# Kernel tuning notes

Measured on AMD Instinct MI355X. Metric: run time of the kernel, lower is better.

The kernel has to match this reference:

```python
import jax, jax.numpy as jnp
import numpy as np

ALPHA = 0.4  # LeakyReLU negative slope used by the GAT


def _gat_head(h, W, a):
    # h: [N, F], W: [F, Fp], a: [2*Fp]; adjacency is all-ones so no masking
    Wh = h @ W                                   # [N, Fp]
    Fp = W.shape[1]
    e = jax.nn.leaky_relu(Wh @ a[:Fp][:, None] + (Wh @ a[Fp:])[None, :], ALPHA)
    att = jax.nn.softmax(e, axis=-1)             # [N, N]
    return att @ Wh                              # [N, Fp]


def _gat(h, W_heads, a_heads, W_gout, a_gout):
    # multi-head GAT: concat elu(head outputs), then single output attention layer
    heads = jax.vmap(_gat_head, in_axes=(None, 0, 0))(h, W_heads, a_heads)  # [H, N, Fp]
    x = jax.nn.elu(heads).transpose(1, 0, 2).reshape(h.shape[0], -1)        # [N, H*Fp]
    return jax.nn.elu(_gat_head(x, W_gout, a_gout))                          # [N, Cg]


def setup_inputs() -> dict:
    key = jax.random.key(0)
    ks = jax.random.split(key, 20)
    bs, R, S = 4, 512, 54
    h, w = 100, 152
    fc_dim, convs_dim4 = 1024, 512
    Cg, H, So = 256, 4, 128
    Fp = Cg // H
    sc = lambda k, shp, s=0.05: jax.random.normal(k, shp, dtype=jnp.float32) * s
    return {
        'region_f': jax.random.normal(ks[0], (bs * R, fc_dim), dtype=jnp.float32),
        'stuff_f': jax.random.normal(ks[1], (bs, convs_dim4, h, w), dtype=jnp.float32),
        'semseg_score': jax.random.normal(ks[2], (bs, S, h, w), dtype=jnp.float32),
        'W_rin': sc(ks[3], (fc_dim, Cg)), 'b_rin': jnp.zeros((Cg,), jnp.float32),
        'W_sin': sc(ks[4], (convs_dim4, Cg)), 'b_sin': jnp.zeros((Cg,), jnp.float32),
        'W_heads': sc(ks[5], (H, Cg, Fp), 0.1), 'a_heads': sc(ks[6], (H, 2 * Fp), 0.1),
        'W_gout': sc(ks[7], (H * Fp, Cg), 0.1), 'a_gout': sc(ks[8], (2 * Cg,), 0.1),
        'W_rout': sc(ks[9], (Cg, Cg)), 'b_rout': jnp.zeros((Cg,), jnp.float32),
        'W_sout': sc(ks[10], (Cg, So)), 'b_sout': jnp.zeros((So,), jnp.float32),
        'W_seg': sc(ks[11], (convs_dim4 + So, S)), 'b_seg': jnp.zeros((S,), jnp.float32),
    }


def reference(region_f, stuff_f, semseg_score,
              W_rin, b_rin, W_sin, b_sin,
              W_heads, a_heads, W_gout, a_gout,
              W_rout, b_rout, W_sout, b_sout,
              W_seg, b_seg):
    bs, Cd, h, w = stuff_f.shape
    S = semseg_score.shape[1]
    R = region_f.shape[0] // bs
    Cg = W_rin.shape[1]

    # node construction
    region_nodes = region_f @ W_rin + b_rin                           # [bs*R, Cg]
    score_flat = semseg_score.reshape(bs, S, h * w)
    class_center = jnp.einsum('bsn,bcn->bsc',
                              jax.nn.softmax(score_flat, axis=-1),
                              stuff_f.reshape(bs, Cd, h * w))          # [bs, S, Cd]
    class_nodes = class_center @ W_sin + b_sin                         # [bs, S, Cg]

    # per-image dense GAT over region + stuff nodes (batched via vmap)
    nodes = jnp.concatenate([region_nodes.reshape(bs, R, Cg), class_nodes], axis=1)
    graph_nodes = jax.vmap(lambda x: _gat(x, W_heads, a_heads, W_gout, a_gout))(nodes)
    new_region, new_class = graph_nodes[:, :R], graph_nodes[:, R:]

    # new box features: concat of original region features and projected graph features
    new_region_f = jnp.concatenate(
        [region_f, new_region.reshape(bs * R, Cg) @ W_rout + b_rout], axis=-1)

    # new stuff features: scatter class nodes back to pixels via class softmax
    new_class_nodes = new_class @ W_sout + b_sout                      # [bs, S, So]
    attn = jax.nn.softmax(score_flat, axis=1)                          # softmax over classes
    new_stuff = jnp.einsum('bsn,bso->bon', attn, new_class_nodes)      # [bs, So, h*w]
    new_stuff = new_stuff.reshape(bs, -1, h, w)

    # 1x1 conv seg head + x4 bilinear upsample (align_corners=False)
    seg_in = jnp.concatenate([stuff_f, new_stuff], axis=1)
    seg = jnp.einsum('bchw,co->bohw', seg_in, W_seg) + b_seg[None, :, None, None]
    segments = jax.image.resize(seg, (bs, S, 4 * h, 4 * w), method='bilinear')
    return new_region_f, segments
```

## Files before the change

### kernel.cpp

```cpp
#include <hip/hip_runtime.h>

#define HW 15200
#define SSD 54
#define NBATCH 4
#define NNODE 566
#define NPAD 576
#define CGD 256
#define CDD 512
#define NSPLIT 25
#define KSPAN 608

typedef __attribute__((ext_vector_type(4))) float f32x4;
typedef __attribute__((ext_vector_type(8))) short bf16x8;
typedef unsigned short ushort_t;

#define BT_RIN   0
#define BT_SIN   262144
#define BT_HEADS 393216
#define BT_GOUT  458752
#define BT_ROUT  524288
#define BT_SOUT  589824
#define BT_SEG2  622592
#define BT_TOTAL 630784

static constexpr long OFF_P     = 0;
static constexpr long OFF_CC    = OFF_P     + (long)NBATCH*SSD*HW;
static constexpr long OFF_NODES = OFF_CC    + (long)NBATCH*64*CDD;
static constexpr long OFF_WH    = OFF_NODES + (long)NBATCH*NNODE*CGD;
static constexpr long OFF_S1    = OFF_WH    + (long)16*NNODE*64;
static constexpr long OFF_S2    = OFF_S1    + 16*NPAD;
static constexpr long OFF_X     = OFF_S2    + 16*NPAD;
static constexpr long OFF_WH2   = OFF_X     + (long)NBATCH*NNODE*CGD;
static constexpr long OFF_S1B   = OFF_WH2   + (long)NBATCH*NNODE*CGD;
static constexpr long OFF_S2B   = OFF_S1B   + NBATCH*NPAD;
static constexpr long OFF_G     = OFF_S2B   + NBATCH*NPAD;
static constexpr long OFF_SUMS  = OFF_G     + (long)NBATCH*NNODE*CGD;
static constexpr long OFF_BT    = OFF_SUMS  + 256;
static constexpr long OFF_ASEG  = OFF_BT    + (BT_TOTAL/2 + 8);
static constexpr long OFF_SEG   = OFF_ASEG  + (long)NBATCH*64*576/2;
static constexpr long OFF_RFB   = OFF_SEG   + (long)NBATCH*SSD*HW;
static constexpr long OFF_WCOMB = OFF_RFB   + 1048576;
static constexpr long OFF_B2    = OFF_WCOMB + 8192;
static constexpr long OFF_ATTNB = OFF_B2    + 64;

__device__ inline float lrelu04(float x){ return x >= 0.f ? x : 0.4f*x; }
__device__ inline float eluf(float x){ return x > 0.f ? x : __expf(x) - 1.f; }
__device__ inline ushort_t f2bf(float f){
    unsigned u = __float_as_uint(f);
    return (ushort_t)((u + 0x7FFFu + ((u >> 16) & 1u)) >> 16);
}
__device__ inline float bf2f(ushort_t u){ return __uint_as_float((unsigned)u << 16); }
__device__ inline bf16x8 pack8(float4 lo, float4 hi){
    union { bf16x8 v; ushort_t u[8]; } p;
    p.u[0]=f2bf(lo.x); p.u[1]=f2bf(lo.y); p.u[2]=f2bf(lo.z); p.u[3]=f2bf(lo.w);
    p.u[4]=f2bf(hi.x); p.u[5]=f2bf(hi.y); p.u[6]=f2bf(hi.z); p.u[7]=f2bf(hi.w);
    return p.v;
}

__global__ __launch_bounds__(512)
void softmax_p(const float* __restrict__ score, ushort_t* __restrict__ pb,
               float* __restrict__ sums, float* __restrict__ s1s2b_zero,
               float* __restrict__ ccp)
{
    int blk = blockIdx.x;
    int t = threadIdx.x;
    if (blk < 256) {
        int b = blk >> 6, s = blk & 63;
        ushort_t* prow = pb + ((long)b*64 + s)*HW;
        if (s >= SSD) {
            for (int i = t; i < HW; i += 512) prow[i] = 0;
            if (t == 0) sums[b*64 + s] = 1.f;
            return;
        }
        const float* row = score + ((long)b*SSD + s)*HW;
        __shared__ float red[8];
        float s_ = 0.f;
        for (int i = t; i < HW; i += 512) {
            float e = __expf(row[i]);
            s_ += e;
            prow[i] = f2bf(e);
        }
        #pragma unroll
        for (int off = 32; off >= 1; off >>= 1) s_ += __shfl_down(s_, off);
        if ((t & 63) == 0) red[t >> 6] = s_;
        __syncthreads();
        if (t == 0) {
            float tot = 0.f;
            #pragma unroll
            for (int u = 0; u < 8; ++u) tot += red[u];
            sums[b*64 + s] = tot;
        }
        return;
    }
    long gid = (long)(blk - 256)*512 + t;
    if (gid < 4608) { s1s2b_zero[gid] = 0.f; return; }
    gid -= 4608;
    if (gid < (long)NBATCH*64*CDD) ccp[gid] = 0.f;
}

__global__ __launch_bounds__(256)
void cc_prep(const ushort_t* __restrict__ pb, const float* __restrict__ stuff,
             ushort_t* __restrict__ sbout, float* __restrict__ ccp,
             const float* __restrict__ score, ushort_t* __restrict__ attnb,
             const float* __restrict__ rf, float* __restrict__ out_region,
             ushort_t* __restrict__ rfb,
             const float* __restrict__ W_seg, ushort_t* __restrict__ asegb,
             const float* __restrict__ W_rin, const float* __restrict__ W_sin,
             const float* __restrict__ W_heads, const float* __restrict__ W_gout,
             const float* __restrict__ W_rout, const float* __restrict__ W_sout,
             const float* __restrict__ b_sout,
             ushort_t* __restrict__ bt, ushort_t* __restrict__ wcomb,
             float* __restrict__ bias2)
{
    int bid = blockIdx.x;
    if (bid < 832) {
        int g = (bid >> 6) * 8 + (bid & 7);
        if (g >= NSPLIT*NBATCH) return;
        int nt = (bid >> 3) & 7;
        int ks = g >> 2, b = g & 3;

        int w = threadIdx.x >> 6, l = threadIdx.x & 63;
        int lr = l & 15, lk = l >> 4;
        int n0 = nt*64 + w*16;
        const ushort_t* Prow = pb + ((long)b*64 + lr)*HW;
        const float*    Srow = stuff + ((long)b*CDD + n0 + lr)*HW;
        ushort_t*       Sout = sbout + ((long)b*CDD + n0 + lr)*HW;
        f32x4 acc[4] = {};
        int kbeg = ks * KSPAN;
        for (int k0 = kbeg; k0 < kbeg + KSPAN; k0 += 32) {
            int kk = k0 + lk*8;
            float4 lo = *(const float4*)&Srow[kk];
            float4 hi = *(const float4*)&Srow[kk + 4];
            bf16x8 bfv = pack8(lo, hi);
            *(bf16x8*)&Sout[kk] = bfv;
            #pragma unroll
            for (int mi = 0; mi < 4; ++mi) {
                bf16x8 af = *(const bf16x8*)&Prow[(long)mi*16*HW + kk];
                acc[mi] = __builtin_amdgcn_mfma_f32_16x16x32_bf16(af, bfv, acc[mi], 0, 0, 0);
            }
        }
        int c = n0 + lr;
        #pragma unroll
        for (int mi = 0; mi < 4; ++mi)
            #pragma unroll
            for (int r = 0; r < 4; ++r) {
                int m = mi*16 + lk*4 + r;
                atomicAdd(&ccp[((long)b*64 + m)*CDD + c], acc[mi][r]);
            }
        return;
    }
    long gid = (long)(bid - 832) * 256 + threadIdx.x;
    if (gid < (long)NBATCH*HW) {
        int b = (int)(gid / HW), n = (int)(gid % HW);
        const float* sp = score + (long)b*SSD*HW + n;
        float v[SSD];
        float m = -1e30f;
        #pragma unroll
        for (int s = 0; s < SSD; ++s) { v[s] = sp[(long)s*HW]; m = fmaxf(m, v[s]); }
        float sum = 0.f;
        #pragma unroll
        for (int s = 0; s < SSD; ++s) { v[s] = __expf(v[s] - m); sum += v[s]; }
        float inv = 1.f / sum;
        ushort_t* ap = attnb + (long)b*64*HW + n;
        #pragma unroll
        for (int s = 0; s < SSD; ++s) ap[(long)s*HW] = f2bf(v[s] * inv);
        #pragma unroll
        for (int s = SSD; s < 64; ++s) ap[(long)s*HW] = 0;
        return;
    }
    gid -= (long)NBATCH*HW;
    if (gid < 524288) {
        long row = gid / 256, col = gid % 256;
        float4 v = reinterpret_cast<const float4*>(rf)[gid];
        reinterpret_cast<float4*>(out_region)[row*320 + col] = v;
        union { ushort_t u[4]; uint2 q; } pk;
        pk.u[0]=f2bf(v.x); pk.u[1]=f2bf(v.y); pk.u[2]=f2bf(v.z); pk.u[3]=f2bf(v.w);
        reinterpret_cast<uint2*>(rfb)[gid] = pk.q;
        return;
    }
    gid -= 524288;
    if (gid < 131072) {
        int b = (int)(gid >> 15);
        int r = (int)(gid & 32767);
        int o = r >> 9, k = r & 511;
        asegb[(long)b*36864 + (long)o*576 + k] = f2bf(o < SSD ? W_seg[k*SSD + o] : 0.f);
        return;
    }
    gid -= 131072;
    if (gid < BT_TOTAL) {
        int i = (int)gid;
        float v;
        if (i < BT_SIN)        { int j=i;            int n=j>>10, k=j&1023; v = W_rin[k*256+n]; }
        else if (i < BT_HEADS) { int j=i-BT_SIN;     int n=j>>9,  k=j&511;  v = W_sin[k*256+n]; }
        else if (i < BT_GOUT)  { int j=i-BT_HEADS;   int h=j>>14, r=j&16383; int f=r>>8, k=r&255;
                                 v = W_heads[(h*256+k)*64+f]; }
        else if (i < BT_ROUT)  { int j=i-BT_GOUT;    int n=j>>8,  k=j&255;  v = W_gout[k*256+n]; }
        else if (i < BT_SOUT)  { int j=i-BT_ROUT;    int n=j>>8,  k=j&255;  v = W_rout[k*256+n]; }
        else if (i < BT_SEG2)  { int j=i-BT_SOUT;    int n=j>>8,  k=j&255;  v = W_sout[k*128+n]; }
        else                   { int j=i-BT_SEG2;    int o=j>>7,  k=j&127;
                                 v = (o < SSD) ? W_seg[(512+k)*SSD + o] : 0.f; }
        bt[i] = f2bf(v);
        return;
    }
    gid -= BT_TOTAL;
    if (gid < 16384) {
        int od = (int)(gid >> 8), k = (int)(gid & 255);
        float v = 0.f;
        if (od < SSD)
            for (int o = 0; o < 128; ++o)
                v += W_sout[k*128 + o] * W_seg[(512+o)*SSD + od];
        wcomb[(long)od*256 + k] = f2bf(v);
        return;
    }
    gid -= 16384;
    if (gid < 64) {
        int od = (int)gid;
        float v = 0.f;
        if (od < SSD)
            for (int o = 0; o < 128; ++o)
                v += b_sout[o] * W_seg[(512+o)*SSD + od];
        bias2[od] = v;
    }
}

template<bool AF32, int OUTMODE>
__device__ __forceinline__
void mm_body(int bx, int by, int bz,
             const void* __restrict__ Ap, const ushort_t* __restrict__ Bt,
             void* __restrict__ Cp, const float* __restrict__ bias,
             int M, int N, int K, int lda, int ldc,
             long sA, int zdivA, long sB, int zmodB, long sC)
{
    int z = bz;
    int w = threadIdx.x >> 6, l = threadIdx.x & 63;
    int lr = l & 15, lk = l >> 4;
    int m0 = bx * 64 + w * 16;
    int n0 = by * 64;
    const ushort_t* bt = Bt + (long)(z % zmodB) * sB;
    int mload = min(m0 + lr, M - 1);
    const float*    Af = (const float*)Ap    + (long)(z / zdivA) * sA + (long)mload * lda;
    const ushort_t* Ab = (const ushort_t*)Ap + (long)(z / zdivA) * sA + (long)mload * lda;
    f32x4 acc[4] = {};

    #pragma unroll 2
    for (int k0 = 0; k0 < K; k0 += 32) {
        int kk = k0 + lk * 8;
        bf16x8 af;
        if (AF32) {
            float4 lo = *(const float4*)&Af[kk];
            float4 hi = *(const float4*)&Af[kk + 4];
            af = pack8(lo, hi);
        } else {
            af = *(const bf16x8*)&Ab[kk];
        }
        #pragma unroll
        for (int j = 0; j < 4; ++j) {
            bf16x8 bf = *(const bf16x8*)&bt[(long)(n0 + j*16 + lr) * K + kk];
            acc[j] = __builtin_amdgcn_mfma_f32_16x16x32_bf16(af, bf, acc[j], 0, 0, 0);
        }
    }

    #pragma unroll
    for (int j = 0; j < 4; ++j) {
        int n = n0 + j*16 + lr;
        float bb = bias ? bias[n] : 0.f;
        #pragma unroll
        for (int r = 0; r < 4; ++r) {
            int m = m0 + lk*4 + r;
            if (OUTMODE == 2) {
                float v = acc[j][r] + bb;
                ((ushort_t*)Cp)[(long)z * sC + (long)n * ldc + m] =
                    (m < M) ? f2bf(v) : (ushort_t)0;
            } else {
                if (m >= M) continue;
                float v = acc[j][r] + bb;
                if (OUTMODE == 0)
                    ((float*)Cp)[(long)z * sC + (long)m * ldc + n] = v;
                else
                    ((ushort_t*)Cp)[(long)z * sC + (long)m * ldc + n] = f2bf(v);
            }
        }
    }
}

__global__ __launch_bounds__(256)
void nodes_both(const ushort_t* __restrict__ rfb, const ushort_t* __restrict__ btRin,
                const float* __restrict__ ccp, const float* __restrict__ sums,
                const ushort_t* __restrict__ btSin, ushort_t* __restrict__ nodes,
                const float* __restrict__ b_rin, const float* __restrict__ b_sin)
{
    if (blockIdx.x < 8) {
        mm_body<false, 1>(blockIdx.x, blockIdx.y, blockIdx.z,
                          rfb, btRin, nodes, b_rin,
                          512, 256, 1024, 1024, 256, 512L*1024, 1, 0, 1, (long)NNODE*CGD);
        return;
    }
    int by = blockIdx.y, bz = blockIdx.z;
    int w = threadIdx.x >> 6, l = threadIdx.x & 63;
    int lr = l & 15, lk = l >> 4;
    int m0 = w * 16, n0 = by * 64;
    int mload = min(m0 + lr, SSD - 1);
    const float* Af = ccp + ((long)bz*64 + mload)*CDD;
    float inv = 1.f / sums[bz*64 + mload];
    f32x4 acc[4] = {};

    #pragma unroll 2
    for (int k0 = 0; k0 < CDD; k0 += 32) {
        int kk = k0 + lk * 8;
        float4 lo = *(const float4*)&Af[kk];
        float4 hi = *(const float4*)&Af[kk + 4];
        lo.x *= inv; lo.y *= inv; lo.z *= inv; lo.w *= inv;
        hi.x *= inv; hi.y *= inv; hi.z *= inv; hi.w *= inv;
        bf16x8 af = pack8(lo, hi);
        #pragma unroll
        for (int j = 0; j < 4; ++j) {
            bf16x8 bf = *(const bf16x8*)&btSin[(long)(n0 + j*16 + lr) * CDD + kk];
            acc[j] = __builtin_amdgcn_mfma_f32_16x16x32_bf16(af, bf, acc[j], 0, 0, 0);
        }
    }

    #pragma unroll
    for (int j = 0; j < 4; ++j) {
        int n = n0 + j*16 + lr;
        float bb = b_sin[n];
        #pragma unroll
        for (int r = 0; r < 4; ++r) {
            int m = m0 + lk*4 + r;
            if (m >= SSD) continue;
            nodes[(long)bz*NNODE*CGD + (long)(512 + m)*CGD + n] = f2bf(acc[j][r] + bb);
        }
    }
}

__global__ __launch_bounds__(256)
void wht_heads(const ushort_t* __restrict__ nodes, const ushort_t* __restrict__ btHeads,
               ushort_t* __restrict__ wht, const float* __restrict__ a_heads,
               float* __restrict__ s1, float* __restrict__ s2)
{
    int bx = blockIdx.x, z = blockIdx.y;
    int w = threadIdx.x >> 6, l = threadIdx.x & 63;
    int lr = l & 15, lk = l >> 4;
    int m0 = bx*64 + w*16;
    const ushort_t* bt = btHeads + (long)(z & 3) * (64L*256);
    int mload = min(m0 + lr, NNODE - 1);
    const ushort_t* Ab = nodes + (long)(z >> 2)*((long)NNODE*CGD) + (long)mload*CGD;
    f32x4 acc[4] = {};

    #pragma unroll 2
    for (int k0 = 0; k0 < 256; k0 += 32) {
        int kk = k0 + lk*8;
        bf16x8 af = *(const bf16x8*)&Ab[kk];
        #pragma unroll
        for (int j = 0; j < 4; ++j) {
            bf16x8 bf = *(const bf16x8*)&bt[(long)(j*16 + lr)*256 + kk];
            acc[j] = __builtin_amdgcn_mfma_f32_16x16x32_bf16(af, bf, acc[j], 0, 0, 0);
        }
    }

    const float* av = a_heads + (long)(z & 3)*128;
    ushort_t* Wout = wht + (long)z*(64L*NPAD);
    float p1[4] = {0.f,0.f,0.f,0.f}, p2[4] = {0.f,0.f,0.f,0.f};
    #pragma unroll
    for (int j = 0; j < 4; ++j) {
        int f = j*16 + lr;
        float c1 = av[f], c2 = av[64 + f];
        #pragma unroll
        for (int r = 0; r < 4; ++r) {
            int m = m0 + lk*4 + r;
            float v = acc[j][r];
            Wout[(long)f*NPAD + m] = (m < NNODE) ? f2bf(v) : (ushort_t)0;
            if (m < NNODE) { p1[r] += v*c1; p2[r] += v*c2; }
        }
    }
    #pragma unroll
    for (int r = 0; r < 4; ++r)
        #pragma unroll
        for (int off = 1; off < 16; off <<= 1) {
            p1[r] += __shfl_xor(p1[r], off);
            p2[r] += __shfl_xor(p2[r], off);
        }
    if (lr == 0) {
        #pragma unroll
        for (int r = 0; r < 4; ++r) {
            int m = m0 + lk*4 + r;
            if (m < NNODE) {
                s1[(long)z*NPAD + m] = p1[r];
                s2[(long)z*NPAD + m] = p2[r];
            }
        }
    }
}

__global__ __launch_bounds__(256)
void wht2_gout(const ushort_t* __restrict__ xbuf, const ushort_t* __restrict__ btGout,
               ushort_t* __restrict__ wht2, const float* __restrict__ a_gout,
               float* __restrict__ s1b, float* __restrict__ s2b)
{
    int bx = blockIdx.x, by = blockIdx.y, z = blockIdx.z;
    int w = threadIdx.x >> 6, l = threadIdx.x & 63;
    int lr = l & 15, lk = l >> 4;
    int m0 = bx*64 + w*16;
    int n0 = by*64;
    int mload = min(m0 + lr, NNODE - 1);
    const ushort_t* Ab = xbuf + (long)z*((long)NNODE*CGD) + (long)mload*CGD;
    f32x4 acc[4] = {};

    #pragma unroll 2
    for (int k0 = 0; k0 < 256; k0 += 32) {
        int kk = k0 + lk*8;
        bf16x8 af = *(const bf16x8*)&Ab[kk];
        #pragma unroll
        for (int j = 0; j < 4; ++j) {
            bf16x8 bf = *(const bf16x8*)&btGout[(long)(n0 + j*16 + lr)*256 + kk];
            acc[j] = __builtin_amdgcn_mfma_f32_16x16x32_bf16(af, bf, acc[j], 0, 0, 0);
        }
    }

    ushort_t* Wout = wht2 + (long)z*(256L*NPAD);
    float p1[4] = {0.f,0.f,0.f,0.f}, p2[4] = {0.f,0.f,0.f,0.f};
    #pragma unroll
    for (int j = 0; j < 4; ++j) {
        int f = n0 + j*16 + lr;
        float c1 = a_gout[f], c2 = a_gout[256 + f];
        #pragma unroll
        for (int r = 0; r < 4; ++r) {
            int m = m0 + lk*4 + r;
            float v = acc[j][r];
            Wout[(long)f*NPAD + m] = (m < NNODE) ? f2bf(v) : (ushort_t)0;
            if (m < NNODE) { p1[r] += v*c1; p2[r] += v*c2; }
        }
    }
    #pragma unroll
    for (int r = 0; r < 4; ++r)
        #pragma unroll
        for (int off = 1; off < 16; off <<= 1) {
            p1[r] += __shfl_xor(p1[r], off);
            p2[r] += __shfl_xor(p2[r], off);
        }
    if (lr == 0) {
        #pragma unroll
        for (int r = 0; r < 4; ++r) {
            int m = m0 + lk*4 + r;
            if (m < NNODE) {
                atomicAdd(&s1b[(long)z*NPAD + m], p1[r]);
                atomicAdd(&s2b[(long)z*NPAD + m], p2[r]);
            }
        }
    }
}

template<int F, int HEADMODE>
__global__ __launch_bounds__(256)
void att_mfma(const ushort_t* __restrict__ WhTall, const float* __restrict__ s1v,
              const float* __restrict__ s2v, ushort_t* __restrict__ outbuf)
{
    constexpr int FT = F / 16;
    int z = blockIdx.y;
    const ushort_t* W  = WhTall + (long)z * F * NPAD;
    const float* s1 = s1v + (long)z * NPAD;
    const float* s2 = s2v + (long)z * NPAD;
    int w = threadIdx.x >> 6, l = threadIdx.x & 63;
    int lr = l & 15, lk = l >> 4;

    __shared__ float s2sh[NPAD];
    __shared__ float redm[4];
    float mxl = -1e30f;
    for (int i = threadIdx.x; i < NPAD; i += 256) {
        float v = (i < NNODE) ? s2[i] : -1e30f;
        s2sh[i] = v;
        mxl = fmaxf(mxl, v);
    }
    #pragma unroll
    for (int off = 32; off >= 1; off >>= 1) mxl = fmaxf(mxl, __shfl_down(mxl, off));
    if (l == 0) redm[w] = mxl;
    __syncthreads();
    float s2max = fmaxf(fmaxf(redm[0], redm[1]), fmaxf(redm[2], redm[3]));

    int m0 = blockIdx.x * 64 + w * 16;
    float s1r = s1[min(m0 + lr, NNODE - 1)];
    float mrow = lrelu04(s1r + s2max);

    union { bf16x8 v; ushort_t u[8]; } onesu;
    #pragma unroll
    for (int u = 0; u < 8; ++u) onesu.u[u] = 0x3F80;
    bf16x8 ones = onesu.v;

    f32x4 acc[FT] = {};
    f32x4 accw = {};

    for (int j0 = 0; j0 < NPAD; j0 += 32) {
        float wv[8];
        #pragma unroll
        for (int u = 0; u < 8; ++u) {
            float e = lrelu04(s1r + s2sh[j0 + lk*8 + u]);
            wv[u] = __expf(e - mrow);
        }
        float4 lo = {wv[0], wv[1], wv[2], wv[3]};
        float4 hi = {wv[4], wv[5], wv[6], wv[7]};
        bf16x8 af = pack8(lo, hi);
        accw = __builtin_amdgcn_mfma_f32_16x16x32_bf16(af, ones, accw, 0, 0, 0);
        #pragma unroll
        for (int ft = 0; ft < FT; ++ft) {
            bf16x8 bf = *(const bf16x8*)&W[(long)(ft*16 + lr)*NPAD + j0 + lk*8];
            acc[ft] = __builtin_amdgcn_mfma_f32_16x16x32_bf16(af, bf, acc[ft], 0, 0, 0);
        }
    }

    #pragma unroll
    for (int r = 0; r < 4; ++r) {
        int m = m0 + lk*4 + r;
        if (m >= NNODE) continue;
        float inv = 1.f / accw[r];
        #pragma unroll
        for (int ft = 0; ft < FT; ++ft) {
            int f = ft*16 + lr;
            float v = eluf(acc[ft][r] * inv);
            if (HEADMODE) {
                int b = z >> 2, h = z & 3;
                outbuf[((long)(b*NNODE + m))*CGD + h*64 + f] = f2bf(v);
            } else {
                outbuf[((long)(z*NNODE + m))*CGD + f] = f2bf(v);
            }
        }
    }
}

__global__ __launch_bounds__(256)
void att_gout_m2(const ushort_t* __restrict__ wht2, const float* __restrict__ s1v,
                 const float* __restrict__ s2v, ushort_t* __restrict__ g,
                 const ushort_t* __restrict__ wcomb, const float* __restrict__ bias2,
                 ushort_t* __restrict__ asegm2)
{
    int bx = blockIdx.x, z = blockIdx.y;
    const ushort_t* W  = wht2 + (long)z * (256L*NPAD);
    const float* s1 = s1v + (long)z * NPAD;
    const float* s2 = s2v + (long)z * NPAD;
    int t = threadIdx.x;
    int w = t >> 6, l = t & 63;
    int lr = l & 15, lk = l >> 4;

    __shared__ float s2sh[NPAD];
    __shared__ float redm[4];
    __shared__ ushort_t gld[64][264];

    float mxl = -1e30f;
    for (int i = t; i < NPAD; i += 256) {
        float v = (i < NNODE) ? s2[i] : -1e30f;
        s2sh[i] = v;
        mxl = fmaxf(mxl, v);
    }
    if (bx == 8)
        for (int i = t; i < 10*264; i += 256) gld[54 + i/264][i%264] = 0;
    #pragma unroll
    for (int off = 32; off >= 1; off >>= 1) mxl = fmaxf(mxl, __shfl_down(mxl, off));
    if (l == 0) redm[w] = mxl;
    __syncthreads();
    float s2max = fmaxf(fmaxf(redm[0], redm[1]), fmaxf(redm[2], redm[3]));

    int m0 = bx * 64 + w * 16;
    float s1r = s1[min(m0 + lr, NNODE - 1)];
    float mrow = lrelu04(s1r + s2max);

    union { bf16x8 v; ushort_t u[8]; } onesu;
    #pragma unroll
    for (int u = 0; u < 8; ++u) onesu.u[u] = 0x3F80;
    bf16x8 ones = onesu.v;

    f32x4 acc[16] = {};
    f32x4 accw = {};

    for (int j0 = 0; j0 < NPAD; j0 += 32) {
        float wv[8];
        #pragma unroll
        for (int u = 0; u < 8; ++u) {
            float e = lrelu04(s1r + s2sh[j0 + lk*8 + u]);
            wv[u] = __expf(e - mrow);
        }
        float4 lo = {wv[0], wv[1], wv[2], wv[3]};
        float4 hi = {wv[4], wv[5], wv[6], wv[7]};
        bf16x8 af = pack8(lo, hi);
        accw = __builtin_amdgcn_mfma_f32_16x16x32_bf16(af, ones, accw, 0, 0, 0);
        #pragma unroll
        for (int ft = 0; ft < 16; ++ft) {
            bf16x8 bf = *(const bf16x8*)&W[(long)(ft*16 + lr)*NPAD + j0 + lk*8];
            acc[ft] = __builtin_amdgcn_mfma_f32_16x16x32_bf16(af, bf, acc[ft], 0, 0, 0);
        }
    }

    #pragma unroll
    for (int r = 0; r < 4; ++r) {
        int m = m0 + lk*4 + r;
        if (m >= NNODE) continue;
        float inv = 1.f / accw[r];
        #pragma unroll
        for (int ft = 0; ft < 16; ++ft) {
            int f = ft*16 + lr;
            ushort_t vb = f2bf(eluf(acc[ft][r] * inv));
            g[((long)(z*NNODE + m))*CGD + f] = vb;
            if (bx == 8) gld[m - 512][f] = vb;
        }
    }

    if (bx == 8) {
        __syncthreads();
        f32x4 acc2[4] = {};
        #pragma unroll 2
        for (int k0 = 0; k0 < 256; k0 += 32) {
            int kk = k0 + lk*8;
            bf16x8 af = *(const bf16x8*)&gld[w*16 + lr][kk];
            #pragma unroll
            for (int j = 0; j < 4; ++j) {
                bf16x8 bf = *(const bf16x8*)&wcomb[(long)(j*16 + lr)*256 + kk];
                acc2[j] = __builtin_amdgcn_mfma_f32_16x16x32_bf16(af, bf, acc2[j], 0, 0, 0);
            }
        }
        #pragma unroll
        for (int j = 0; j < 4; ++j) {
            int n = j*16 + lr;
            float bb = bias2[n];
            #pragma unroll
            for (int r = 0; r < 4; ++r) {
                int m = w*16 + lk*4 + r;
                asegm2[(long)z*36864 + (long)n*576 + m] =
                    (m < SSD) ? f2bf(acc2[j][r] + bb) : (ushort_t)0;
            }
        }
    }
}

__device__ __forceinline__
void seg_body(int nt, int b,
              const ushort_t* __restrict__ stuffb, const ushort_t* __restrict__ attnb,
              const ushort_t* __restrict__ asegb, const float* __restrict__ b_seg,
              float* __restrict__ seg)
{
    int w = threadIdx.x >> 6, l = threadIdx.x & 63;
    int lr = l & 15, lk = l >> 4;
    int n0 = nt*128 + w*32;
    const ushort_t* A = asegb + (long)b*36864;
    const ushort_t* S = stuffb + (long)b*CDD*HW;
    const ushort_t* T = attnb + (long)b*64*HW;
    f32x4 acc[4][2] = {};
    int n1 = min(n0 + lr, HW-1);
    int n2 = min(n0 + 16 + lr, HW-1);

    for (int k0 = 0; k0 < 576; k0 += 32) {
        const ushort_t* Bsrc = (k0 < 512) ? S + (long)k0*HW : T + (long)(k0-512)*HW;
        long kb = (long)(lk*8)*HW;
        union { bf16x8 v; ushort_t u[8]; } b0, b1;
        #pragma unroll
        for (int u = 0; u < 8; ++u) {
            b0.u[u] = Bsrc[kb + (long)u*HW + n1];
            b1.u[u] = Bsrc[kb + (long)u*HW + n2];
        }
        #pragma unroll
        for (int ot = 0; ot < 4; ++ot) {
            bf16x8 af = *(const bf16x8*)&A[(ot*16 + lr)*576 + k0 + lk*8];
            acc[ot][0] = __builtin_amdgcn_mfma_f32_16x16x32_bf16(af, b0.v, acc[ot][0], 0,0,0);
            acc[ot][1] = __builtin_amdgcn_mfma_f32_16x16x32_bf16(af, b1.v, acc[ot][1], 0,0,0);
        }
    }

    #pragma unroll
    for (int ot = 0; ot < 4; ++ot) {
        #pragma unroll
        for (int r = 0; r < 4; ++r) {
            int o = ot*16 + lk*4 + r;
            if (o >= SSD) continue;
            float bb = b_seg[o];
            int na = n0 + lr, nb = n0 + 16 + lr;
            if (na < HW) seg[((long)b*SSD + o)*HW + na] = acc[ot][0][r] + bb;
            if (nb < HW) seg[((long)b*SSD + o)*HW + nb] = acc[ot][1][r] + bb;
        }
    }
}

__global__ __launch_bounds__(256)
void rout_seg(const ushort_t* __restrict__ g_bf, const ushort_t* __restrict__ btRout,
              float* __restrict__ outreg, const float* __restrict__ b_rout,
              const ushort_t* __restrict__ stuffb, const ushort_t* __restrict__ attnb,
              const ushort_t* __restrict__ asegb, const float* __restrict__ b_seg,
              float* __restrict__ segb)
{
    int bid = blockIdx.x;
    if (bid < 128) {
        int x = bid & 7, y = (bid >> 3) & 3, z = bid >> 5;
        mm_body<false, 0>(x, y, z, g_bf, btRout, outreg, b_rout,
                          512, 256, 256, 256, 1280, (long)NNODE*CGD, 1, 0, 1, 512L*1280);
    } else {
        int sid = bid - 128;
        seg_body(sid % 119, sid / 119, stuffb, attnb, asegb, b_seg, segb);
    }
}

__global__ __launch_bounds__(256)
void resize_v2_kernel(const float* __restrict__ seg, float* __restrict__ out)
{
    long u = (long)blockIdx.x * 256 + threadIdx.x;
    const long TOT4 = (long)NBATCH * SSD * 400 * 152;
    if (u >= TOT4) return;
    int m = (int)(u % 152);
    long r = u / 152;
    int y = (int)(r % 400);
    long c = r / 400;
    float fy = y * 0.25f - 0.375f;
    int y0 = (int)floorf(fy);
    float wy = fy - (float)y0;
    int y0c = max(y0, 0), y1c = min(y0 + 1, 99);
    const float* sp = seg + c * HW;
    int xm = max(m - 1, 0), xp = min(m + 1, 151);
    float r0a = sp[y0c * 152 + xm], r0b = sp[y0c * 152 + m], r0c = sp[y0c * 152 + xp];
    float r1a = sp[y1c * 152 + xm], r1b = sp[y1c * 152 + m], r1c = sp[y1c * 152 + xp];
    float ra = r0a + wy * (r1a - r0a);
    float rb = r0b + wy * (r1b - r0b);
    float rc = r0c + wy * (r1c - r0c);
    float4 o4;
    o4.x = 0.375f * ra + 0.625f * rb;
    o4.y = 0.125f * ra + 0.875f * rb;
    o4.z = 0.875f * rb + 0.125f * rc;
    o4.w = 0.625f * rb + 0.375f * rc;
    reinterpret_cast<float4*>(out)[u] = o4;
}

extern "C" void kernel_launch(void* const* d_in, const int* in_sizes, int n_in,
                              void* d_out, int out_size, void* d_ws, size_t ws_size,
                              hipStream_t stream)
{
    const float* region_f = (const float*)d_in[0];
    const float* stuff    = (const float*)d_in[1];
    const float* score    = (const float*)d_in[2];
    const float* W_rin    = (const float*)d_in[3];
    const float* b_rin    = (const float*)d_in[4];
    const float* W_sin    = (const float*)d_in[5];
    const float* b_sin    = (const float*)d_in[6];
    const float* W_heads  = (const float*)d_in[7];
    const float* a_heads  = (const float*)d_in[8];
    const float* W_gout   = (const float*)d_in[9];
    const float* a_gout   = (const float*)d_in[10];
    const float* W_rout   = (const float*)d_in[11];
    const float* b_rout   = (const float*)d_in[12];
    const float* W_sout   = (const float*)d_in[13];
    const float* b_sout   = (const float*)d_in[14];
    const float* W_seg    = (const float*)d_in[15];
    const float* b_seg    = (const float*)d_in[16];

    float* out = (float*)d_out;
    float* ws  = (float*)d_ws;

    ushort_t* pb   = (ushort_t*)(ws + OFF_P);
    float* ccp     = ws + OFF_CC;
    ushort_t* nodes_bf = (ushort_t*)(ws + OFF_NODES);
    ushort_t* wht  = (ushort_t*)(ws + OFF_WH);
    float* s1      = ws + OFF_S1;
    float* s2      = ws + OFF_S2;
    ushort_t* xbuf_bf = (ushort_t*)(ws + OFF_X);
    ushort_t* wht2 = (ushort_t*)(ws + OFF_WH2);
    float* s1b     = ws + OFF_S1B;
    float* s2b     = ws + OFF_S2B;
    ushort_t* g_bf = (ushort_t*)(ws + OFF_G);
    float* sums    = ws + OFF_SUMS;
    ushort_t* bt   = (ushort_t*)(ws + OFF_BT);
    ushort_t* asegb = (ushort_t*)(ws + OFF_ASEG);
    float* segb    = ws + OFF_SEG;
    ushort_t* rfb  = (ushort_t*)(ws + OFF_RFB);
    ushort_t* wcomb = (ushort_t*)(ws + OFF_WCOMB);
    float* bias2v  = ws + OFF_B2;
    ushort_t* attnb = (ushort_t*)(ws + OFF_ATTNB);

    float* out_region = out;
    float* out_seg    = out + 2048L*1280;
    ushort_t* stuffb  = (ushort_t*)out_seg;

    softmax_p<<<521, 512, 0, stream>>>(score, pb, sums, s1b, ccp);

    cc_prep<<<6158, 256, 0, stream>>>(pb, stuff, stuffb, ccp, score, attnb,
                                      region_f, out_region, rfb, W_seg, asegb,
                                      W_rin, W_sin, W_heads, W_gout, W_rout, W_sout,
                                      b_sout, bt, wcomb, bias2v);

    nodes_both<<<dim3(9, 4, 4), 256, 0, stream>>>(
        rfb, bt + BT_RIN, ccp, sums, bt + BT_SIN, nodes_bf, b_rin, b_sin);

    wht_heads<<<dim3(9, 16), 256, 0, stream>>>(
        nodes_bf, bt + BT_HEADS, wht, a_heads, s1, s2);

    att_mfma<64, 1><<<dim3(9, 16), 256, 0, stream>>>(wht, s1, s2, xbuf_bf);

    wht2_gout<<<dim3(9, 4, 4), 256, 0, stream>>>(
        xbuf_bf, bt + BT_GOUT, wht2, a_gout, s1b, s2b);

    att_gout_m2<<<dim3(9, 4), 256, 0, stream>>>(
        wht2, s1b, s2b, g_bf, wcomb, bias2v, asegb + 512);

    rout_seg<<<604, 256, 0, stream>>>(
        g_bf, bt + BT_ROUT, out_region + 1024, b_rout,
        stuffb, attnb, asegb, b_seg, segb);

    resize_v2_kernel<<<((long)NBATCH*SSD*400*152 + 255)/256, 256, 0, stream>>>(segb, out_seg);
}
```

Baseline: 315.8 us.

## Split seg GEMM over K and overlap stuff part with small GAT kernels

The segmentation 1x1-conv GEMM is split into a K=512 part over the stuff features, which does not depend on the graph, and a K=64 part over the attention features, which needs the graph output. The 476 K=512 tiles are spread as extra blocks across the five small GAT kernels, so they fill otherwise idle CUs. The final kernel now only adds the K=64 contribution with a read-modify-write into seg. The risk is extra seg traffic from the accumulate pass, and the seg tiles could delay the latency-critical GAT blocks.

```diff
diff --git a/kernel.cpp b/kernel.cpp
--- a/kernel.cpp
+++ b/kernel.cpp
@@ -223,6 +223,98 @@
     }
 }
 
+__device__ __forceinline__
+void seg512_body(int nt, int b,
+                 const ushort_t* __restrict__ stuffb,
+                 const ushort_t* __restrict__ asegb, const float* __restrict__ b_seg,
+                 float* __restrict__ seg)
+{
+    int w = threadIdx.x >> 6, l = threadIdx.x & 63;
+    int lr = l & 15, lk = l >> 4;
+    int n0 = nt*128 + w*32;
+    const ushort_t* A = asegb + (long)b*36864;
+    const ushort_t* S = stuffb + (long)b*CDD*HW;
+    f32x4 acc[4][2] = {};
+    int n1 = min(n0 + lr, HW-1);
+    int n2 = min(n0 + 16 + lr, HW-1);
+
+    for (int k0 = 0; k0 < 512; k0 += 32) {
+        const ushort_t* Bsrc = S + (long)k0*HW;
+        long kb = (long)(lk*8)*HW;
+        union { bf16x8 v; ushort_t u[8]; } b0, b1;
+        #pragma unroll
+        for (int u = 0; u < 8; ++u) {
+            b0.u[u] = Bsrc[kb + (long)u*HW + n1];
+            b1.u[u] = Bsrc[kb + (long)u*HW + n2];
+        }
+        #pragma unroll
+        for (int ot = 0; ot < 4; ++ot) {
+            bf16x8 af = *(const bf16x8*)&A[(ot*16 + lr)*576 + k0 + lk*8];
+            acc[ot][0] = __builtin_amdgcn_mfma_f32_16x16x32_bf16(af, b0.v, acc[ot][0], 0,0,0);
+            acc[ot][1] = __builtin_amdgcn_mfma_f32_16x16x32_bf16(af, b1.v, acc[ot][1], 0,0,0);
+        }
+    }
+
+    #pragma unroll
+    for (int ot = 0; ot < 4; ++ot) {
+        #pragma unroll
+        for (int r = 0; r < 4; ++r) {
+            int o = ot*16 + lk*4 + r;
+            if (o >= SSD) continue;
+            float bb = b_seg[o];
+            int na = n0 + lr, nb = n0 + 16 + lr;
+            if (na < HW) seg[((long)b*SSD + o)*HW + na] = acc[ot][0][r] + bb;
+            if (nb < HW) seg[((long)b*SSD + o)*HW + nb] = acc[ot][1][r] + bb;
+        }
+    }
+}
+
+__device__ __forceinline__
+void segk64_body(int nt, int b,
+                 const ushort_t* __restrict__ attnb,
+                 const ushort_t* __restrict__ asegb,
+                 float* __restrict__ seg)
+{
+    int w = threadIdx.x >> 6, l = threadIdx.x & 63;
+    int lr = l & 15, lk = l >> 4;
+    int n0 = nt*128 + w*32;
+    const ushort_t* A = asegb + (long)b*36864;
+    const ushort_t* T = attnb + (long)b*64*HW;
+    f32x4 acc[4][2] = {};
+    int n1 = min(n0 + lr, HW-1);
+    int n2 = min(n0 + 16 + lr, HW-1);
+
+    #pragma unroll
+    for (int k0 = 512; k0 < 576; k0 += 32) {
+        const ushort_t* Bsrc = T + (long)(k0-512)*HW;
+        long kb = (long)(lk*8)*HW;
+        union { bf16x8 v; ushort_t u[8]; } b0, b1;
+        #pragma unroll
+        for (int u = 0; u < 8; ++u) {
+            b0.u[u] = Bsrc[kb + (long)u*HW + n1];
+            b1.u[u] = Bsrc[kb + (long)u*HW + n2];
+        }
+        #pragma unroll
+        for (int ot = 0; ot < 4; ++ot) {
+            bf16x8 af = *(const bf16x8*)&A[(ot*16 + lr)*576 + k0 + lk*8];
+            acc[ot][0] = __builtin_amdgcn_mfma_f32_16x16x32_bf16(af, b0.v, acc[ot][0], 0,0,0);
+            acc[ot][1] = __builtin_amdgcn_mfma_f32_16x16x32_bf16(af, b1.v, acc[ot][1], 0,0,0);
+        }
+    }
+
+    #pragma unroll
+    for (int ot = 0; ot < 4; ++ot) {
+        #pragma unroll
+        for (int r = 0; r < 4; ++r) {
+            int o = ot*16 + lk*4 + r;
+            if (o >= SSD) continue;
+            int na = n0 + lr, nb = n0 + 16 + lr;
+            if (na < HW) { long i = ((long)b*SSD + o)*HW + na; seg[i] += acc[ot][0][r]; }
+            if (nb < HW) { long i = ((long)b*SSD + o)*HW + nb; seg[i] += acc[ot][1][r]; }
+        }
+    }
+}
+
 template<bool AF32, int OUTMODE>
 __device__ __forceinline__
 void mm_body(int bx, int by, int bz,
@@ -284,18 +376,25 @@
 }
 
 __global__ __launch_bounds__(256)
-void nodes_both(const ushort_t* __restrict__ rfb, const ushort_t* __restrict__ btRin,
-                const float* __restrict__ ccp, const float* __restrict__ sums,
-                const ushort_t* __restrict__ btSin, ushort_t* __restrict__ nodes,
-                const float* __restrict__ b_rin, const float* __restrict__ b_sin)
-{
-    if (blockIdx.x < 8) {
-        mm_body<false, 1>(blockIdx.x, blockIdx.y, blockIdx.z,
-                          rfb, btRin, nodes, b_rin,
+void nodes_seg(const ushort_t* __restrict__ rfb, const ushort_t* __restrict__ btRin,
+               const float* __restrict__ ccp, const float* __restrict__ sums,
+               const ushort_t* __restrict__ btSin, ushort_t* __restrict__ nodes,
+               const float* __restrict__ b_rin, const float* __restrict__ b_sin,
+               const ushort_t* __restrict__ stuffb, const ushort_t* __restrict__ asegb,
+               const float* __restrict__ b_seg, float* __restrict__ segb)
+{
+    int bid = blockIdx.x;
+    if (bid >= 144) {
+        int sid = bid - 144;
+        seg512_body(sid % 119, sid / 119, stuffb, asegb, b_seg, segb);
+        return;
+    }
+    int bx = bid % 9, by = (bid/9) % 4, bz = bid / 36;
+    if (bx < 8) {
+        mm_body<false, 1>(bx, by, bz, rfb, btRin, nodes, b_rin,
                           512, 256, 1024, 1024, 256, 512L*1024, 1, 0, 1, (long)NNODE*CGD);
         return;
     }
-    int by = blockIdx.y, bz = blockIdx.z;
     int w = threadIdx.x >> 6, l = threadIdx.x & 63;
     int lr = l & 15, lk = l >> 4;
     int m0 = w * 16, n0 = by * 64;
@@ -333,11 +432,19 @@
 }
 
 __global__ __launch_bounds__(256)
-void wht_heads(const ushort_t* __restrict__ nodes, const ushort_t* __restrict__ btHeads,
-               ushort_t* __restrict__ wht, const float* __restrict__ a_heads,
-               float* __restrict__ s1, float* __restrict__ s2)
-{
-    int bx = blockIdx.x, z = blockIdx.y;
+void wht_seg(const ushort_t* __restrict__ nodes, const ushort_t* __restrict__ btHeads,
+             ushort_t* __restrict__ wht, const float* __restrict__ a_heads,
+             float* __restrict__ s1, float* __restrict__ s2,
+             const ushort_t* __restrict__ stuffb, const ushort_t* __restrict__ asegb,
+             const float* __restrict__ b_seg, float* __restrict__ segb)
+{
+    int bid = blockIdx.x;
+    if (bid >= 144) {
+        int sid = bid - 144 + 80;
+        seg512_body(sid % 119, sid / 119, stuffb, asegb, b_seg, segb);
+        return;
+    }
+    int bx = bid % 9, z = bid / 9;
     int w = threadIdx.x >> 6, l = threadIdx.x & 63;
     int lr = l & 15, lk = l >> 4;
     int m0 = bx*64 + w*16;
@@ -391,71 +498,13 @@
     }
 }
 
-__global__ __launch_bounds__(256)
-void wht2_gout(const ushort_t* __restrict__ xbuf, const ushort_t* __restrict__ btGout,
-               ushort_t* __restrict__ wht2, const float* __restrict__ a_gout,
-               float* __restrict__ s1b, float* __restrict__ s2b)
-{
-    int bx = blockIdx.x, by = blockIdx.y, z = blockIdx.z;
-    int w = threadIdx.x >> 6, l = threadIdx.x & 63;
-    int lr = l & 15, lk = l >> 4;
-    int m0 = bx*64 + w*16;
-    int n0 = by*64;
-    int mload = min(m0 + lr, NNODE - 1);
-    const ushort_t* Ab = xbuf + (long)z*((long)NNODE*CGD) + (long)mload*CGD;
-    f32x4 acc[4] = {};
-
-    #pragma unroll 2
-    for (int k0 = 0; k0 < 256; k0 += 32) {
-        int kk = k0 + lk*8;
-        bf16x8 af = *(const bf16x8*)&Ab[kk];
-        #pragma unroll
-        for (int j = 0; j < 4; ++j) {
-            bf16x8 bf = *(const bf16x8*)&btGout[(long)(n0 + j*16 + lr)*256 + kk];
-            acc[j] = __builtin_amdgcn_mfma_f32_16x16x32_bf16(af, bf, acc[j], 0, 0, 0);
-        }
-    }
-
-    ushort_t* Wout = wht2 + (long)z*(256L*NPAD);
-    float p1[4] = {0.f,0.f,0.f,0.f}, p2[4] = {0.f,0.f,0.f,0.f};
-    #pragma unroll
-    for (int j = 0; j < 4; ++j) {
-        int f = n0 + j*16 + lr;
-        float c1 = a_gout[f], c2 = a_gout[256 + f];
-        #pragma unroll
-        for (int r = 0; r < 4; ++r) {
-            int m = m0 + lk*4 + r;
-            float v = acc[j][r];
-            Wout[(long)f*NPAD + m] = (m < NNODE) ? f2bf(v) : (ushort_t)0;
-            if (m < NNODE) { p1[r] += v*c1; p2[r] += v*c2; }
-        }
-    }
-    #pragma unroll
-    for (int r = 0; r < 4; ++r)
-        #pragma unroll
-        for (int off = 1; off < 16; off <<= 1) {
-            p1[r] += __shfl_xor(p1[r], off);
-            p2[r] += __shfl_xor(p2[r], off);
-        }
-    if (lr == 0) {
-        #pragma unroll
-        for (int r = 0; r < 4; ++r) {
-            int m = m0 + lk*4 + r;
-            if (m < NNODE) {
-                atomicAdd(&s1b[(long)z*NPAD + m], p1[r]);
-                atomicAdd(&s2b[(long)z*NPAD + m], p2[r]);
-            }
-        }
-    }
-}
-
 template<int F, int HEADMODE>
-__global__ __launch_bounds__(256)
-void att_mfma(const ushort_t* __restrict__ WhTall, const float* __restrict__ s1v,
-              const float* __restrict__ s2v, ushort_t* __restrict__ outbuf)
+__device__ __forceinline__
+void att_body(int bx, int z, const ushort_t* __restrict__ WhTall,
+              const float* __restrict__ s1v, const float* __restrict__ s2v,
+              ushort_t* __restrict__ outbuf)
 {
     constexpr int FT = F / 16;
-    int z = blockIdx.y;
     const ushort_t* W  = WhTall + (long)z * F * NPAD;
     const float* s1 = s1v + (long)z * NPAD;
     const float* s2 = s2v + (long)z * NPAD;
@@ -476,7 +525,7 @@
     __syncthreads();
     float s2max = fmaxf(fmaxf(redm[0], redm[1]), fmaxf(redm[2], redm[3]));
 
-    int m0 = blockIdx.x * 64 + w * 16;
+    int m0 = bx * 64 + w * 16;
     float s1r = s1[min(m0 + lr, NNODE - 1)];
     float mrow = lrelu04(s1r + s2max);
 
@@ -526,12 +575,101 @@
 }
 
 __global__ __launch_bounds__(256)
-void att_gout_m2(const ushort_t* __restrict__ wht2, const float* __restrict__ s1v,
-                 const float* __restrict__ s2v, ushort_t* __restrict__ g,
-                 const ushort_t* __restrict__ wcomb, const float* __restrict__ bias2,
-                 ushort_t* __restrict__ asegm2)
-{
-    int bx = blockIdx.x, z = blockIdx.y;
+void att64_seg(const ushort_t* __restrict__ wht, const float* __restrict__ s1,
+               const float* __restrict__ s2, ushort_t* __restrict__ xbuf,
+               const ushort_t* __restrict__ stuffb, const ushort_t* __restrict__ asegb,
+               const float* __restrict__ b_seg, float* __restrict__ segb)
+{
+    int bid = blockIdx.x;
+    if (bid >= 144) {
+        int sid = bid - 144 + 160;
+        seg512_body(sid % 119, sid / 119, stuffb, asegb, b_seg, segb);
+        return;
+    }
+    att_body<64, 1>(bid % 9, bid / 9, wht, s1, s2, xbuf);
+}
+
+__global__ __launch_bounds__(256)
+void wht2_seg(const ushort_t* __restrict__ xbuf, const ushort_t* __restrict__ btGout,
+              ushort_t* __restrict__ wht2, const float* __restrict__ a_gout,
+              float* __restrict__ s1b, float* __restrict__ s2b,
+              const ushort_t* __restrict__ stuffb, const ushort_t* __restrict__ asegb,
+              const float* __restrict__ b_seg, float* __restrict__ segb)
+{
+    int bid = blockIdx.x;
+    if (bid >= 144) {
+        int sid = bid - 144 + 240;
+        seg512_body(sid % 119, sid / 119, stuffb, asegb, b_seg, segb);
+        return;
+    }
+    int bx = bid % 9, by = (bid/9) % 4, z = bid / 36;
+    int w = threadIdx.x >> 6, l = threadIdx.x & 63;
+    int lr = l & 15, lk = l >> 4;
+    int m0 = bx*64 + w*16;
+    int n0 = by*64;
+    int mload = min(m0 + lr, NNODE - 1);
+    const ushort_t* Ab = xbuf + (long)z*((long)NNODE*CGD) + (long)mload*CGD;
+    f32x4 acc[4] = {};
+
+    #pragma unroll 2
+    for (int k0 = 0; k0 < 256; k0 += 32) {
+        int kk = k0 + lk*8;
+        bf16x8 af = *(const bf16x8*)&Ab[kk];
+        #pragma unroll
+        for (int j = 0; j < 4; ++j) {
+            bf16x8 bf = *(const bf16x8*)&btGout[(long)(n0 + j*16 + lr)*256 + kk];
+            acc[j] = __builtin_amdgcn_mfma_f32_16x16x32_bf16(af, bf, acc[j], 0, 0, 0);
+        }
+    }
+
+    ushort_t* Wout = wht2 + (long)z*(256L*NPAD);
+    float p1[4] = {0.f,0.f,0.f,0.f}, p2[4] = {0.f,0.f,0.f,0.f};
+    #pragma unroll
+    for (int j = 0; j < 4; ++j) {
+        int f = n0 + j*16 + lr;
+        float c1 = a_gout[f], c2 = a_gout[256 + f];
+        #pragma unroll
+        for (int r = 0; r < 4; ++r) {
+            int m = m0 + lk*4 + r;
+            float v = acc[j][r];
+            Wout[(long)f*NPAD + m] = (m < NNODE) ? f2bf(v) : (ushort_t)0;
+            if (m < NNODE) { p1[r] += v*c1; p2[r] += v*c2; }
+        }
+    }
+    #pragma unroll
+    for (int r = 0; r < 4; ++r)
+        #pragma unroll
+        for (int off = 1; off < 16; off <<= 1) {
+            p1[r] += __shfl_xor(p1[r], off);
+            p2[r] += __shfl_xor(p2[r], off);
+        }
+    if (lr == 0) {
+        #pragma unroll
+        for (int r = 0; r < 4; ++r) {
+            int m = m0 + lk*4 + r;
+            if (m < NNODE) {
+                atomicAdd(&s1b[(long)z*NPAD + m], p1[r]);
+                atomicAdd(&s2b[(long)z*NPAD + m], p2[r]);
+            }
+        }
+    }
+}
+
+__global__ __launch_bounds__(256)
+void attg_seg(const ushort_t* __restrict__ wht2, const float* __restrict__ s1v,
+              const float* __restrict__ s2v, ushort_t* __restrict__ g,
+              const ushort_t* __restrict__ wcomb, const float* __restrict__ bias2,
+              ushort_t* __restrict__ asegm2,
+              const ushort_t* __restrict__ stuffb, const ushort_t* __restrict__ asegb,
+              const float* __restrict__ b_seg, float* __restrict__ segb)
+{
+    int bid = blockIdx.x;
+    if (bid >= 36) {
+        int sid = bid - 36 + 320;
+        seg512_body(sid % 119, sid / 119, stuffb, asegb, b_seg, segb);
+        return;
+    }
+    int bx = bid % 9, z = bid / 9;
     const ushort_t* W  = wht2 + (long)z * (256L*NPAD);
     const float* s1 = s1v + (long)z * NPAD;
     const float* s2 = s2v + (long)z * NPAD;
@@ -628,59 +766,11 @@
     }
 }
 
-__device__ __forceinline__
-void seg_body(int nt, int b,
-              const ushort_t* __restrict__ stuffb, const ushort_t* __restrict__ attnb,
-              const ushort_t* __restrict__ asegb, const float* __restrict__ b_seg,
-              float* __restrict__ seg)
-{
-    int w = threadIdx.x >> 6, l = threadIdx.x & 63;
-    int lr = l & 15, lk = l >> 4;
-    int n0 = nt*128 + w*32;
-    const ushort_t* A = asegb + (long)b*36864;
-    const ushort_t* S = stuffb + (long)b*CDD*HW;
-    const ushort_t* T = attnb + (long)b*64*HW;
-    f32x4 acc[4][2] = {};
-    int n1 = min(n0 + lr, HW-1);
-    int n2 = min(n0 + 16 + lr, HW-1);
-
-    for (int k0 = 0; k0 < 576; k0 += 32) {
-        const ushort_t* Bsrc = (k0 < 512) ? S + (long)k0*HW : T + (long)(k0-512)*HW;
-        long kb = (long)(lk*8)*HW;
-        union { bf16x8 v; ushort_t u[8]; } b0, b1;
-        #pragma unroll
-        for (int u = 0; u < 8; ++u) {
-            b0.u[u] = Bsrc[kb + (long)u*HW + n1];
-            b1.u[u] = Bsrc[kb + (long)u*HW + n2];
-        }
-        #pragma unroll
-        for (int ot = 0; ot < 4; ++ot) {
-            bf16x8 af = *(const bf16x8*)&A[(ot*16 + lr)*576 + k0 + lk*8];
-            acc[ot][0] = __builtin_amdgcn_mfma_f32_16x16x32_bf16(af, b0.v, acc[ot][0], 0,0,0);
-            acc[ot][1] = __builtin_amdgcn_mfma_f32_16x16x32_bf16(af, b1.v, acc[ot][1], 0,0,0);
-        }
-    }
-
-    #pragma unroll
-    for (int ot = 0; ot < 4; ++ot) {
-        #pragma unroll
-        for (int r = 0; r < 4; ++r) {
-            int o = ot*16 + lk*4 + r;
-            if (o >= SSD) continue;
-            float bb = b_seg[o];
-            int na = n0 + lr, nb = n0 + 16 + lr;
-            if (na < HW) seg[((long)b*SSD + o)*HW + na] = acc[ot][0][r] + bb;
-            if (nb < HW) seg[((long)b*SSD + o)*HW + nb] = acc[ot][1][r] + bb;
-        }
-    }
-}
-
 __global__ __launch_bounds__(256)
-void rout_seg(const ushort_t* __restrict__ g_bf, const ushort_t* __restrict__ btRout,
-              float* __restrict__ outreg, const float* __restrict__ b_rout,
-              const ushort_t* __restrict__ stuffb, const ushort_t* __restrict__ attnb,
-              const ushort_t* __restrict__ asegb, const float* __restrict__ b_seg,
-              float* __restrict__ segb)
+void rout_segk(const ushort_t* __restrict__ g_bf, const ushort_t* __restrict__ btRout,
+               float* __restrict__ outreg, const float* __restrict__ b_rout,
+               const ushort_t* __restrict__ attnb, const ushort_t* __restrict__ asegb,
+               float* __restrict__ segb)
 {
     int bid = blockIdx.x;
     if (bid < 128) {
@@ -689,7 +779,7 @@
                           512, 256, 256, 256, 1280, (long)NNODE*CGD, 1, 0, 1, 512L*1280);
     } else {
         int sid = bid - 128;
-        seg_body(sid % 119, sid / 119, stuffb, attnb, asegb, b_seg, segb);
+        segk64_body(sid % 119, sid / 119, attnb, asegb, segb);
     }
 }
 
@@ -778,23 +868,27 @@
                                       W_rin, W_sin, W_heads, W_gout, W_rout, W_sout,
                                       b_sout, bt, wcomb, bias2v);
 
-    nodes_both<<<dim3(9, 4, 4), 256, 0, stream>>>(
-        rfb, bt + BT_RIN, ccp, sums, bt + BT_SIN, nodes_bf, b_rin, b_sin);
-
-    wht_heads<<<dim3(9, 16), 256, 0, stream>>>(
-        nodes_bf, bt + BT_HEADS, wht, a_heads, s1, s2);
-
-    att_mfma<64, 1><<<dim3(9, 16), 256, 0, stream>>>(wht, s1, s2, xbuf_bf);
-
-    wht2_gout<<<dim3(9, 4, 4), 256, 0, stream>>>(
-        xbuf_bf, bt + BT_GOUT, wht2, a_gout, s1b, s2b);
-
-    att_gout_m2<<<dim3(9, 4), 256, 0, stream>>>(
-        wht2, s1b, s2b, g_bf, wcomb, bias2v, asegb + 512);
-
-    rout_seg<<<604, 256, 0, stream>>>(
-        g_bf, bt + BT_ROUT, out_region + 1024, b_rout,
-        stuffb, attnb, asegb, b_seg, segb);
+    nodes_seg<<<224, 256, 0, stream>>>(
+        rfb, bt + BT_RIN, ccp, sums, bt + BT_SIN, nodes_bf, b_rin, b_sin,
+        stuffb, asegb, b_seg, segb);
+
+    wht_seg<<<224, 256, 0, stream>>>(
+        nodes_bf, bt + BT_HEADS, wht, a_heads, s1, s2,
+        stuffb, asegb, b_seg, segb);
+
+    att64_seg<<<224, 256, 0, stream>>>(
+        wht, s1, s2, xbuf_bf, stuffb, asegb, b_seg, segb);
+
+    wht2_seg<<<224, 256, 0, stream>>>(
+        xbuf_bf, bt + BT_GOUT, wht2, a_gout, s1b, s2b,
+        stuffb, asegb, b_seg, segb);
+
+    attg_seg<<<192, 256, 0, stream>>>(
+        wht2, s1b, s2b, g_bf, wcomb, bias2v, asegb + 512,
+        stuffb, asegb, b_seg, segb);
+
+    rout_segk<<<604, 256, 0, stream>>>(
+        g_bf, bt + BT_ROUT, out_region + 1024, b_rout, attnb, asegb, segb);
 
     resize_v2_kernel<<<((long)NBATCH*SSD*400*152 + 255)/256, 256, 0, stream>>>(segb, out_seg);
 }
```

Measured after the change: 282.7 us. 1.12x faster.
